# Optimization experiments

Measured on AMD Instinct MI355X. Metric: run time of the kernel, lower is better.

## Reference

```python
import jax, jax.numpy as jnp
import numpy as np

B, T, DIN, H = 32, 4096, 256, 256


def _log_g(x):
    # log of g(x) = where(x>=0, x+0.5, sigmoid(x)), computed stably in log space
    return jnp.where(x >= 0.0, jnp.log(jax.nn.relu(x) + 0.5), -jax.nn.softplus(-x))


def setup_inputs() -> dict:
    key = jax.random.key(0)
    ks = jax.random.split(key, 4)
    scale = (6.0 / (DIN + H)) ** 0.5  # xavier_uniform
    return {
        "x": jax.random.normal(ks[0], (B, T, DIN), dtype=jnp.float32),
        "h0": jax.random.normal(ks[1], (B, 1, H), dtype=jnp.float32),
        "Wz": jax.random.uniform(ks[2], (H, DIN), jnp.float32, -scale, scale),
        "bz": jnp.zeros((H,), jnp.float32),
        "Wh": jax.random.uniform(ks[3], (H, DIN), jnp.float32, -scale, scale),
        "bh": jnp.zeros((H,), jnp.float32),
    }


def reference(x, h0, Wz, bz, Wh, bh):
    # minGRU training path: log-space parallel scan (Heinsen scan)
    k = jnp.einsum("bti,hi->bth", x, Wz) + bz            # pre-activation of z gate
    log_z = -jax.nn.softplus(-k)                           # log sigmoid(k)
    log_coeffs = -jax.nn.softplus(k)                       # log(1 - sigmoid(k))
    log_h0 = _log_g(h0)                                    # (B,1,H)
    log_tilde_h = _log_g(jnp.einsum("bti,hi->bth", x, Wh) + bh)
    log_values = jnp.concatenate([log_h0, log_z + log_tilde_h], axis=1)  # (B,T+1,H)
    # a_star[t] = sum_{s<=t} log_coeffs[s], with a leading zero
    a_star = jnp.cumsum(jnp.pad(log_coeffs, ((0, 0), (1, 0), (0, 0))), axis=1)
    # logcumsumexp along time via associative scan with logaddexp
    lcse = jax.lax.associative_scan(jnp.logaddexp, log_values - a_star, axis=1)
    log_h = a_star + lcse                                  # (B,T+1,H)
    return jnp.exp(log_h[:, 1:])                           # (B,T,H)
```

## Files before the change

kernel.cpp:

```cpp
#include <hip/hip_runtime.h>
#include <hip/hip_fp16.h>

typedef __attribute__((ext_vector_type(8))) short short8;
typedef __attribute__((ext_vector_type(4))) float f32x4;
typedef unsigned short ushort_t;
typedef unsigned int uint_t;

#define B_SZ 32
#define T_SZ 4096
#define D_IN 256
#define H_SZ 256
#define M_SZ (B_SZ * T_SZ)
#define CHUNK 64
#define NCHUNK (T_SZ / CHUNK)

__device__ __forceinline__ ushort_t f2bf(float f) {
  unsigned int u = __float_as_uint(f);
  unsigned int r = (u + 0x7FFFu + ((u >> 16) & 1u)) >> 16;
  return (ushort_t)r;
}

__device__ __forceinline__ float sigmoidf_(float xv) {
  float e = __expf(-fabsf(xv));
  float s = 1.0f / (1.0f + e);
  return xv >= 0.0f ? s : 1.0f - s;
}

__device__ __forceinline__ float unpack_lo(uint_t pk) {
  return __half2float(__ushort_as_half((ushort_t)(pk & 0xFFFFu)));
}
__device__ __forceinline__ float unpack_hi(uint_t pk) {
  return __half2float(__ushort_as_half((ushort_t)(pk >> 16)));
}

__global__ void prep_w(const float* __restrict__ Wz, const float* __restrict__ Wh,
                       ushort_t* __restrict__ wsB) {
  int g = blockIdx.x * 256 + threadIdx.x;
  if (g >= 8 * 2048) return;
  int ks = g >> 11;
  int r = g & 2047;
  int c = r >> 9;
  int n = r & 511;
  int h = (n >> 5) * 16 + (n & 15);
  const float* W = ((n >> 4) & 1) ? Wh : Wz;
  const float* src = W + (size_t)h * D_IN + ks * 32 + c * 8;
  ushort_t* dst = wsB + (size_t)g * 8;
#pragma unroll
  for (int j = 0; j < 8; ++j) dst[j] = f2bf(src[j]);
}

__global__ __launch_bounds__(512, 4) void gemm_av(
    const float* __restrict__ x, const ushort_t* __restrict__ wsB,
    const float* __restrict__ bz, const float* __restrict__ bh,
    uint_t* __restrict__ av) {
  __shared__ __align__(16) unsigned char lds[73728];
  ushort_t* As = (ushort_t*)lds;
  ushort_t* Bs = (ushort_t*)(lds + 8192);

  const int tid = threadIdx.x;
  const int lane = tid & 63;
  const int wid = tid >> 6;
  const int m0 = blockIdx.x * 64;

  const int a_row = tid & 63;
  const int a_g = tid >> 6;
  const float* asrc = x + (size_t)(m0 + a_row) * D_IN + a_g * 8;

  f32x4 acc[4][4];
#pragma unroll
  for (int rt = 0; rt < 4; ++rt)
#pragma unroll
    for (int ct = 0; ct < 4; ++ct) {
      f32x4 z4 = {0.f, 0.f, 0.f, 0.f};
      acc[rt][ct] = z4;
    }

  {
    const ushort_t* bsrc = wsB + (size_t)wid * 2048 + lane * 8;
    ushort_t* bdst = Bs + wid * 2048;
#pragma unroll
    for (int cc = 0; cc < 4; ++cc) {
      __builtin_amdgcn_global_load_lds(
          (const __attribute__((address_space(1))) void*)(bsrc + cc * 512),
          (__attribute__((address_space(3))) void*)(bdst + cc * 512), 16, 0, 0);
    }
    if (tid < 256) {
      float4 f0 = *(const float4*)(asrc);
      float4 f1 = *(const float4*)(asrc + 4);
      short8 vfr;
      ushort_t* vp = (ushort_t*)&vfr;
      vp[0] = f2bf(f0.x); vp[1] = f2bf(f0.y); vp[2] = f2bf(f0.z); vp[3] = f2bf(f0.w);
      vp[4] = f2bf(f1.x); vp[5] = f2bf(f1.y); vp[6] = f2bf(f1.z); vp[7] = f2bf(f1.w);
      *(short8*)(As + tid * 8) = vfr;
    }
  }
  __syncthreads();

#pragma unroll
  for (int ks = 0; ks < 8; ++ks) {
    const int cur = ks & 1;
    short8 afr[4], bfr[4];
    {
      const int c = lane >> 4;
      const int r16 = lane & 15;
#pragma unroll
      for (int rt = 0; rt < 4; ++rt) {
        int row = rt * 16 + r16;
        afr[rt] = *(const short8*)(As + cur * 2048 + (c * 64 + row) * 8);
      }
#pragma unroll
      for (int ct = 0; ct < 4; ++ct) {
        int n = wid * 64 + ct * 16 + r16;
        bfr[ct] = *(const short8*)(Bs + cur * 16384 + (c * 512 + n) * 8);
      }
    }
    float4 nf0, nf1;
    if (ks < 7) {
      const ushort_t* bsrc = wsB + (size_t)(ks + 1) * 16384 + wid * 2048 + lane * 8;
      ushort_t* bdst = Bs + (cur ^ 1) * 16384 + wid * 2048;
#pragma unroll
      for (int cc = 0; cc < 4; ++cc) {
        __builtin_amdgcn_global_load_lds(
            (const __attribute__((address_space(1))) void*)(bsrc + cc * 512),
            (__attribute__((address_space(3))) void*)(bdst + cc * 512), 16, 0, 0);
      }
      if (tid < 256) {
        nf0 = *(const float4*)(asrc + (ks + 1) * 32);
        nf1 = *(const float4*)(asrc + (ks + 1) * 32 + 4);
      }
    }
#pragma unroll
    for (int rt = 0; rt < 4; ++rt)
#pragma unroll
      for (int ct = 0; ct < 4; ++ct)
        acc[rt][ct] = __builtin_amdgcn_mfma_f32_16x16x32_bf16(
            afr[rt], bfr[ct], acc[rt][ct], 0, 0, 0);
    if (ks < 7 && tid < 256) {
      short8 vfr;
      ushort_t* vp = (ushort_t*)&vfr;
      vp[0] = f2bf(nf0.x); vp[1] = f2bf(nf0.y); vp[2] = f2bf(nf0.z); vp[3] = f2bf(nf0.w);
      vp[4] = f2bf(nf1.x); vp[5] = f2bf(nf1.y); vp[6] = f2bf(nf1.z); vp[7] = f2bf(nf1.w);
      *(short8*)(As + (cur ^ 1) * 2048 + tid * 8) = vfr;
    }
    __syncthreads();
  }

  const int col16 = lane & 15;
  const int rgrp = lane >> 4;
#pragma unroll
  for (int i = 0; i < 2; ++i) {
    int hh = (wid * 2 + i) * 16 + col16;
    float bzv = bz[hh];
    float bhv = bh[hh];
#pragma unroll
    for (int rt = 0; rt < 4; ++rt) {
#pragma unroll
      for (int j = 0; j < 4; ++j) {
        int row = m0 + rt * 16 + rgrp * 4 + j;
        float kv = acc[rt][2 * i][j] + bzv;
        float pv = acc[rt][2 * i + 1][j] + bhv;
        float a = sigmoidf_(-kv);
        float z = 1.0f - a;
        float gg = (pv >= 0.0f) ? (pv + 0.5f) : sigmoidf_(pv);
        float vv = z * gg;
        uint_t pk = (uint_t)__half_as_ushort(__float2half_rn(a)) |
                    ((uint_t)__half_as_ushort(__float2half_rn(vv)) << 16);
        av[(size_t)row * H_SZ + hh] = pk;
      }
    }
  }
}

__global__ __launch_bounds__(256) void chunk_reduce(
    const uint_t* __restrict__ av, float2* __restrict__ cAV) {
  const int b = blockIdx.x >> 6;
  const int c = blockIdx.x & 63;
  const int h = threadIdx.x;
  const uint_t* p = av + ((size_t)b * T_SZ + c * CHUNK) * H_SZ + h;

  uint_t buf[CHUNK];
#pragma unroll
  for (int s = 0; s < CHUNK; ++s) buf[s] = p[(size_t)s * H_SZ];

  float A = 1.0f, V = 0.0f;
#pragma unroll
  for (int s = 0; s < CHUNK; ++s) {
    float a = unpack_lo(buf[s]);
    float v = unpack_hi(buf[s]);
    A = a * A;
    V = fmaf(a, V, v);
  }
  float2 r; r.x = A; r.y = V;
  cAV[((size_t)b * NCHUNK + c) * H_SZ + h] = r;
}

__global__ __launch_bounds__(256) void chunk_carry(
    const float* __restrict__ h0, const float2* __restrict__ cAV,
    float* __restrict__ hb) {
  const int b = blockIdx.x;
  const int h = threadIdx.x;
  float v0 = h0[b * H_SZ + h];
  float hc = (v0 >= 0.0f) ? (v0 + 0.5f) : sigmoidf_(v0);

  const float2* p = cAV + (size_t)b * NCHUNK * H_SZ + h;
  float* o = hb + (size_t)b * NCHUNK * H_SZ + h;

  float2 buf[NCHUNK];
#pragma unroll
  for (int c = 0; c < NCHUNK; ++c) buf[c] = p[(size_t)c * H_SZ];

#pragma unroll
  for (int c = 0; c < NCHUNK; ++c) {
    o[(size_t)c * H_SZ] = hc;
    hc = fmaf(buf[c].x, hc, buf[c].y);
  }
}

__global__ __launch_bounds__(256) void chunk_scan_out(
    const uint_t* av, const float* __restrict__ hb, float* out) {
  const int b = blockIdx.x >> 6;
  const int c = blockIdx.x & 63;
  const int h = threadIdx.x;

  float hc = hb[((size_t)b * NCHUNK + c) * H_SZ + h];
  const uint_t* p = av + ((size_t)b * T_SZ + c * CHUNK) * H_SZ + h;
  float* o = out + ((size_t)b * T_SZ + c * CHUNK) * H_SZ + h;

  uint_t buf[CHUNK];
#pragma unroll
  for (int s = 0; s < CHUNK; ++s) buf[s] = p[(size_t)s * H_SZ];

#pragma unroll
  for (int s = 0; s < CHUNK; ++s) {
    float a = unpack_lo(buf[s]);
    float v = unpack_hi(buf[s]);
    hc = fmaf(a, hc, v);
    o[(size_t)s * H_SZ] = hc;
  }
}

__global__ __launch_bounds__(64) void scan_seq(const float* __restrict__ h0,
                                               const uint_t* av, float* out) {
  const int b = blockIdx.x >> 2;
  const int hg = blockIdx.x & 3;
  const int h = hg * 64 + threadIdx.x;

  float v0 = h0[b * H_SZ + h];
  float hc = (v0 >= 0.0f) ? (v0 + 0.5f) : sigmoidf_(v0);

  const uint_t* p = av + (size_t)b * T_SZ * H_SZ + h;
  float* o = out + (size_t)b * T_SZ * H_SZ + h;

  uint_t buf[32];
#pragma unroll
  for (int d = 0; d < 32; ++d) buf[d] = p[(size_t)d * H_SZ];

  for (int t0 = 0; t0 < T_SZ; t0 += 32) {
#pragma unroll
    for (int d = 0; d < 32; ++d) {
      int t = t0 + d;
      uint_t pk = buf[d];
      int tn = t + 32;
      if (tn < T_SZ) buf[d] = p[(size_t)tn * H_SZ];
      hc = fmaf(unpack_lo(pk), hc, unpack_hi(pk));
      o[(size_t)t * H_SZ] = hc;
    }
  }
}

extern "C" void kernel_launch(void* const* d_in, const int* in_sizes, int n_in,
                              void* d_out, int out_size, void* d_ws, size_t ws_size,
                              hipStream_t stream) {
  const float* x  = (const float*)d_in[0];
  const float* h0 = (const float*)d_in[1];
  const float* Wz = (const float*)d_in[2];
  const float* bz = (const float*)d_in[3];
  const float* Wh = (const float*)d_in[4];
  const float* bh = (const float*)d_in[5];
  float* out = (float*)d_out;

  const size_t wsBBytes = 262144;
  const size_t cavBytes = (size_t)B_SZ * NCHUNK * H_SZ * 8;
  const size_t hbBytes  = (size_t)B_SZ * NCHUNK * H_SZ * 4;
  const size_t avOff    = 8388608;
  const size_t avBytes  = (size_t)M_SZ * H_SZ * 4;

  ushort_t* wsB = (ushort_t*)d_ws;
  float2* cAV = (float2*)((char*)d_ws + wsBBytes);
  float* hb   = (float*)((char*)d_ws + wsBBytes + cavBytes);

  const bool haveSummaries = ws_size >= wsBBytes + cavBytes + hbBytes;
  uint_t* av;
  if (ws_size >= avOff + avBytes) {
    av = (uint_t*)((char*)d_ws + avOff);
  } else {
    av = (uint_t*)d_out;
  }

  prep_w<<<64, 256, 0, stream>>>(Wz, Wh, wsB);
  gemm_av<<<M_SZ / 64, 512, 0, stream>>>(x, wsB, bz, bh, av);
  if (haveSummaries) {
    chunk_reduce<<<B_SZ * NCHUNK, 256, 0, stream>>>(av, cAV);
    chunk_carry<<<B_SZ, 256, 0, stream>>>(h0, cAV, hb);
    chunk_scan_out<<<B_SZ * NCHUNK, 256, 0, stream>>>(av, hb, out);
  } else {
    scan_seq<<<B_SZ * 4, 64, 0, stream>>>(h0, av, out);
  }
}
```

Baseline: 174.7 us.

## Keep weights in registers and stream fp32 x tiles via swizzled LDS

The GEMM kernel now loads each wave's full bf16 weight slice into registers once per block and processes four 64-row chunks per block, so the weight tile is no longer restaged through LDS for every 64-row tile. Raw fp32 x rows are copied straight into a double-buffered, XOR-swizzled LDS buffer with global_load_lds, and the bf16 conversion happens at fragment-read time. prep_w is relaid out to match the per-lane register fragment order. This cuts weight traffic and per-tile setup, at the cost of heavy register use (occupancy hint lowered to 2), 128KB of LDS per block, and redundant conversion of x per wave.

```diff
diff --git a/kernel.cpp b/kernel.cpp
--- a/kernel.cpp
+++ b/kernel.cpp
@@ -13,6 +13,8 @@
 #define M_SZ (B_SZ * T_SZ)
 #define CHUNK 64
 #define NCHUNK (T_SZ / CHUNK)
+#define NC_PER_BLK 4
+#define GEMM_GRID (M_SZ / (NC_PER_BLK * CHUNK))
 
 __device__ __forceinline__ ushort_t f2bf(float f) {
   unsigned int u = __float_as_uint(f);
@@ -36,138 +38,126 @@
 __global__ void prep_w(const float* __restrict__ Wz, const float* __restrict__ Wh,
                        ushort_t* __restrict__ wsB) {
   int g = blockIdx.x * 256 + threadIdx.x;
-  if (g >= 8 * 2048) return;
-  int ks = g >> 11;
-  int r = g & 2047;
-  int c = r >> 9;
-  int n = r & 511;
-  int h = (n >> 5) * 16 + (n & 15);
-  const float* W = ((n >> 4) & 1) ? Wh : Wz;
-  const float* src = W + (size_t)h * D_IN + ks * 32 + c * 8;
+  if (g >= 32 * 8 * 64) return;
+  int lane = g & 63;
+  int ks = (g >> 6) & 7;
+  int grp = g >> 9;
+  int c16 = lane & 15;
+  int h = (grp >> 1) * 16 + c16;
+  int k0 = ks * 32 + (lane >> 4) * 8;
+  const float* W = (grp & 1) ? Wh : Wz;
+  const float* src = W + (size_t)h * D_IN + k0;
   ushort_t* dst = wsB + (size_t)g * 8;
 #pragma unroll
   for (int j = 0; j < 8; ++j) dst[j] = f2bf(src[j]);
 }
 
-__global__ __launch_bounds__(512, 4) void gemm_av(
+__global__ __launch_bounds__(512, 2) void gemm_av(
     const float* __restrict__ x, const ushort_t* __restrict__ wsB,
     const float* __restrict__ bz, const float* __restrict__ bh,
     uint_t* __restrict__ av) {
-  __shared__ __align__(16) unsigned char lds[73728];
-  ushort_t* As = (ushort_t*)lds;
-  ushort_t* Bs = (ushort_t*)(lds + 8192);
+  __shared__ __align__(16) float ldsA[2 * CHUNK * D_IN];
 
   const int tid = threadIdx.x;
   const int lane = tid & 63;
   const int wid = tid >> 6;
-  const int m0 = blockIdx.x * 64;
-
-  const int a_row = tid & 63;
-  const int a_g = tid >> 6;
-  const float* asrc = x + (size_t)(m0 + a_row) * D_IN + a_g * 8;
-
-  f32x4 acc[4][4];
-#pragma unroll
-  for (int rt = 0; rt < 4; ++rt)
-#pragma unroll
-    for (int ct = 0; ct < 4; ++ct) {
-      f32x4 z4 = {0.f, 0.f, 0.f, 0.f};
-      acc[rt][ct] = z4;
-    }
-
-  {
-    const ushort_t* bsrc = wsB + (size_t)wid * 2048 + lane * 8;
-    ushort_t* bdst = Bs + wid * 2048;
-#pragma unroll
-    for (int cc = 0; cc < 4; ++cc) {
-      __builtin_amdgcn_global_load_lds(
-          (const __attribute__((address_space(1))) void*)(bsrc + cc * 512),
-          (__attribute__((address_space(3))) void*)(bdst + cc * 512), 16, 0, 0);
-    }
-    if (tid < 256) {
-      float4 f0 = *(const float4*)(asrc);
-      float4 f1 = *(const float4*)(asrc + 4);
-      short8 vfr;
-      ushort_t* vp = (ushort_t*)&vfr;
-      vp[0] = f2bf(f0.x); vp[1] = f2bf(f0.y); vp[2] = f2bf(f0.z); vp[3] = f2bf(f0.w);
-      vp[4] = f2bf(f1.x); vp[5] = f2bf(f1.y); vp[6] = f2bf(f1.z); vp[7] = f2bf(f1.w);
-      *(short8*)(As + tid * 8) = vfr;
-    }
-  }
-  __syncthreads();
-
-#pragma unroll
-  for (int ks = 0; ks < 8; ++ks) {
-    const int cur = ks & 1;
-    short8 afr[4], bfr[4];
-    {
-      const int c = lane >> 4;
-      const int r16 = lane & 15;
-#pragma unroll
-      for (int rt = 0; rt < 4; ++rt) {
-        int row = rt * 16 + r16;
-        afr[rt] = *(const short8*)(As + cur * 2048 + (c * 64 + row) * 8);
-      }
-#pragma unroll
-      for (int ct = 0; ct < 4; ++ct) {
-        int n = wid * 64 + ct * 16 + r16;
-        bfr[ct] = *(const short8*)(Bs + cur * 16384 + (c * 512 + n) * 8);
-      }
-    }
-    float4 nf0, nf1;
-    if (ks < 7) {
-      const ushort_t* bsrc = wsB + (size_t)(ks + 1) * 16384 + wid * 2048 + lane * 8;
-      ushort_t* bdst = Bs + (cur ^ 1) * 16384 + wid * 2048;
-#pragma unroll
-      for (int cc = 0; cc < 4; ++cc) {
-        __builtin_amdgcn_global_load_lds(
-            (const __attribute__((address_space(1))) void*)(bsrc + cc * 512),
-            (__attribute__((address_space(3))) void*)(bdst + cc * 512), 16, 0, 0);
-      }
-      if (tid < 256) {
-        nf0 = *(const float4*)(asrc + (ks + 1) * 32);
-        nf1 = *(const float4*)(asrc + (ks + 1) * 32 + 4);
-      }
-    }
-#pragma unroll
-    for (int rt = 0; rt < 4; ++rt)
-#pragma unroll
-      for (int ct = 0; ct < 4; ++ct)
-        acc[rt][ct] = __builtin_amdgcn_mfma_f32_16x16x32_bf16(
-            afr[rt], bfr[ct], acc[rt][ct], 0, 0, 0);
-    if (ks < 7 && tid < 256) {
-      short8 vfr;
-      ushort_t* vp = (ushort_t*)&vfr;
-      vp[0] = f2bf(nf0.x); vp[1] = f2bf(nf0.y); vp[2] = f2bf(nf0.z); vp[3] = f2bf(nf0.w);
-      vp[4] = f2bf(nf1.x); vp[5] = f2bf(nf1.y); vp[6] = f2bf(nf1.z); vp[7] = f2bf(nf1.w);
-      *(short8*)(As + (cur ^ 1) * 2048 + tid * 8) = vfr;
-    }
-    __syncthreads();
-  }
-
   const int col16 = lane & 15;
   const int rgrp = lane >> 4;
+  const size_t rowBase = (size_t)blockIdx.x * (NC_PER_BLK * CHUNK);
+
+  short8 bfr[4][8];
+#pragma unroll
+  for (int ct = 0; ct < 4; ++ct)
+#pragma unroll
+    for (int ks = 0; ks < 8; ++ks)
+      bfr[ct][ks] =
+          *(const short8*)(wsB + ((size_t)(((wid * 4 + ct) * 8 + ks) * 64 + lane)) * 8);
+
+  float bzv[2], bhv[2];
 #pragma unroll
   for (int i = 0; i < 2; ++i) {
     int hh = (wid * 2 + i) * 16 + col16;
-    float bzv = bz[hh];
-    float bhv = bh[hh];
-#pragma unroll
-    for (int rt = 0; rt < 4; ++rt) {
-#pragma unroll
-      for (int j = 0; j < 4; ++j) {
-        int row = m0 + rt * 16 + rgrp * 4 + j;
-        float kv = acc[rt][2 * i][j] + bzv;
-        float pv = acc[rt][2 * i + 1][j] + bhv;
-        float a = sigmoidf_(-kv);
-        float z = 1.0f - a;
-        float gg = (pv >= 0.0f) ? (pv + 0.5f) : sigmoidf_(pv);
-        float vv = z * gg;
-        uint_t pk = (uint_t)__half_as_ushort(__float2half_rn(a)) |
-                    ((uint_t)__half_as_ushort(__float2half_rn(vv)) << 16);
-        av[(size_t)row * H_SZ + hh] = pk;
+    bzv[i] = bz[hh];
+    bhv[i] = bh[hh];
+  }
+
+  auto STAGE = [&](int cc) {
+    const char* xbase = (const char*)(x + (rowBase + (size_t)cc * CHUNK) * D_IN);
+    const int soff = (lane * 16) ^ (wid << 4);
+    char* lbase = (char*)&ldsA[(cc & 1) * (CHUNK * D_IN)];
+#pragma unroll
+    for (int q = 0; q < 8; ++q) {
+      const int r = q * 8 + wid;
+      __builtin_amdgcn_global_load_lds(
+          (const __attribute__((address_space(1))) void*)(xbase + (size_t)r * 1024 + soff),
+          (__attribute__((address_space(3))) void*)(lbase + r * 1024), 16, 0, 0);
+    }
+  };
+
+  STAGE(0);
+  __syncthreads();
+
+  const int koffsw = (rgrp * 32) ^ ((lane & 7) << 4);
+
+#pragma unroll 1
+  for (int cc = 0; cc < NC_PER_BLK; ++cc) {
+    if (cc + 1 < NC_PER_BLK) STAGE(cc + 1);
+
+    const char* Ab = (const char*)&ldsA[(cc & 1) * (CHUNK * D_IN)];
+
+    f32x4 acc[4][4];
+#pragma unroll
+    for (int rt = 0; rt < 4; ++rt)
+#pragma unroll
+      for (int ct = 0; ct < 4; ++ct) {
+        f32x4 z4 = {0.f, 0.f, 0.f, 0.f};
+        acc[rt][ct] = z4;
       }
-    }
+
+#pragma unroll
+    for (int ks = 0; ks < 8; ++ks) {
+#pragma unroll
+      for (int rt = 0; rt < 4; ++rt) {
+        const int row = rt * 16 + col16;
+        const int a1 = row * 1024 + ks * 128 + koffsw;
+        float4 f0 = *(const float4*)(Ab + a1);
+        float4 f1 = *(const float4*)(Ab + (a1 ^ 16));
+        union { ushort_t e[8]; short8 s; } cv;
+        cv.e[0] = f2bf(f0.x); cv.e[1] = f2bf(f0.y);
+        cv.e[2] = f2bf(f0.z); cv.e[3] = f2bf(f0.w);
+        cv.e[4] = f2bf(f1.x); cv.e[5] = f2bf(f1.y);
+        cv.e[6] = f2bf(f1.z); cv.e[7] = f2bf(f1.w);
+        short8 afr = cv.s;
+#pragma unroll
+        for (int ct = 0; ct < 4; ++ct)
+          acc[rt][ct] = __builtin_amdgcn_mfma_f32_16x16x32_bf16(
+              afr, bfr[ct][ks], acc[rt][ct], 0, 0, 0);
+      }
+    }
+
+    const size_t crow0 = rowBase + (size_t)cc * CHUNK;
+#pragma unroll
+    for (int i = 0; i < 2; ++i) {
+      const int hh = (wid * 2 + i) * 16 + col16;
+#pragma unroll
+      for (int rt = 0; rt < 4; ++rt) {
+#pragma unroll
+        for (int j = 0; j < 4; ++j) {
+          float kv = acc[rt][2 * i][j] + bzv[i];
+          float pv = acc[rt][2 * i + 1][j] + bhv[i];
+          float a = sigmoidf_(-kv);
+          float z = 1.0f - a;
+          float gg = (pv >= 0.0f) ? (pv + 0.5f) : sigmoidf_(pv);
+          float vv = z * gg;
+          int row = rt * 16 + rgrp * 4 + j;
+          uint_t pk = (uint_t)__half_as_ushort(__float2half_rn(a)) |
+                      ((uint_t)__half_as_ushort(__float2half_rn(vv)) << 16);
+          av[(crow0 + row) * H_SZ + hh] = pk;
+        }
+      }
+    }
+
+    __syncthreads();
   }
 }
 
@@ -298,7 +288,7 @@
   }
 
   prep_w<<<64, 256, 0, stream>>>(Wz, Wh, wsB);
-  gemm_av<<<M_SZ / 64, 512, 0, stream>>>(x, wsB, bz, bh, av);
+  gemm_av<<<GEMM_GRID, 512, 0, stream>>>(x, wsB, bz, bh, av);
   if (haveSummaries) {
     chunk_reduce<<<B_SZ * NCHUNK, 256, 0, stream>>>(av, cAV);
     chunk_carry<<<B_SZ, 256, 0, stream>>>(h0, cAV, hb);
```

After: 186.6 us. 1.07x slower.

## Load pre-swizzled weight fragments directly into registers instead of staging through LDS

Applied to the files above, without the earlier changes.

The weight prep kernel now writes the bf16 weights in MFMA fragment order per wave, lane and k-step. The GEMM kernel then reads each B fragment with one coalesced 16-byte global load straight into registers, double-buffered across k-steps. This removes the 64KB LDS B buffer and the LDS read traffic, shrinking shared memory from 72KB to 8KB so more blocks can be resident. The cost is that every block re-fetches weights from L2 through the vector path and uses more registers per thread.

```diff
diff --git a/kernel.cpp b/kernel.cpp
--- a/kernel.cpp
+++ b/kernel.cpp
@@ -36,14 +36,15 @@
 __global__ void prep_w(const float* __restrict__ Wz, const float* __restrict__ Wh,
                        ushort_t* __restrict__ wsB) {
   int g = blockIdx.x * 256 + threadIdx.x;
-  if (g >= 8 * 2048) return;
-  int ks = g >> 11;
-  int r = g & 2047;
-  int c = r >> 9;
-  int n = r & 511;
-  int h = (n >> 5) * 16 + (n & 15);
-  const float* W = ((n >> 4) & 1) ? Wh : Wz;
-  const float* src = W + (size_t)h * D_IN + ks * 32 + c * 8;
+  if (g >= 32 * 8 * 64) return;
+  int lane = g & 63;
+  int ks = (g >> 6) & 7;
+  int grp = g >> 9;
+  int c16 = lane & 15;
+  int h = (grp >> 1) * 16 + c16;
+  int k0 = ks * 32 + (lane >> 4) * 8;
+  const float* W = (grp & 1) ? Wh : Wz;
+  const float* src = W + (size_t)h * D_IN + k0;
   ushort_t* dst = wsB + (size_t)g * 8;
 #pragma unroll
   for (int j = 0; j < 8; ++j) dst[j] = f2bf(src[j]);
@@ -53,9 +54,8 @@
     const float* __restrict__ x, const ushort_t* __restrict__ wsB,
     const float* __restrict__ bz, const float* __restrict__ bh,
     uint_t* __restrict__ av) {
-  __shared__ __align__(16) unsigned char lds[73728];
+  __shared__ __align__(16) unsigned char lds[8192];
   ushort_t* As = (ushort_t*)lds;
-  ushort_t* Bs = (ushort_t*)(lds + 8192);
 
   const int tid = threadIdx.x;
   const int lane = tid & 63;
@@ -66,6 +66,8 @@
   const int a_g = tid >> 6;
   const float* asrc = x + (size_t)(m0 + a_row) * D_IN + a_g * 8;
 
+  const short8* bgr = (const short8*)wsB;
+
   f32x4 acc[4][4];
 #pragma unroll
   for (int rt = 0; rt < 4; ++rt)
@@ -75,23 +77,21 @@
       acc[rt][ct] = z4;
     }
 
+  short8 bfr[2][4];
+
   {
-    const ushort_t* bsrc = wsB + (size_t)wid * 2048 + lane * 8;
-    ushort_t* bdst = Bs + wid * 2048;
-#pragma unroll
-    for (int cc = 0; cc < 4; ++cc) {
-      __builtin_amdgcn_global_load_lds(
-          (const __attribute__((address_space(1))) void*)(bsrc + cc * 512),
-          (__attribute__((address_space(3))) void*)(bdst + cc * 512), 16, 0, 0);
-    }
+#pragma unroll
+    for (int ct = 0; ct < 4; ++ct)
+      bfr[0][ct] = bgr[((wid * 4 + ct) * 8 + 0) * 64 + lane];
     if (tid < 256) {
       float4 f0 = *(const float4*)(asrc);
       float4 f1 = *(const float4*)(asrc + 4);
-      short8 vfr;
-      ushort_t* vp = (ushort_t*)&vfr;
-      vp[0] = f2bf(f0.x); vp[1] = f2bf(f0.y); vp[2] = f2bf(f0.z); vp[3] = f2bf(f0.w);
-      vp[4] = f2bf(f1.x); vp[5] = f2bf(f1.y); vp[6] = f2bf(f1.z); vp[7] = f2bf(f1.w);
-      *(short8*)(As + tid * 8) = vfr;
+      union { ushort_t e[8]; short8 s; } cv;
+      cv.e[0] = f2bf(f0.x); cv.e[1] = f2bf(f0.y);
+      cv.e[2] = f2bf(f0.z); cv.e[3] = f2bf(f0.w);
+      cv.e[4] = f2bf(f1.x); cv.e[5] = f2bf(f1.y);
+      cv.e[6] = f2bf(f1.z); cv.e[7] = f2bf(f1.w);
+      *(short8*)(As + tid * 8) = cv.s;
     }
   }
   __syncthreads();
@@ -99,7 +99,7 @@
 #pragma unroll
   for (int ks = 0; ks < 8; ++ks) {
     const int cur = ks & 1;
-    short8 afr[4], bfr[4];
+    short8 afr[4];
     {
       const int c = lane >> 4;
       const int r16 = lane & 15;
@@ -108,22 +108,12 @@
         int row = rt * 16 + r16;
         afr[rt] = *(const short8*)(As + cur * 2048 + (c * 64 + row) * 8);
       }
-#pragma unroll
-      for (int ct = 0; ct < 4; ++ct) {
-        int n = wid * 64 + ct * 16 + r16;
-        bfr[ct] = *(const short8*)(Bs + cur * 16384 + (c * 512 + n) * 8);
-      }
     }
     float4 nf0, nf1;
     if (ks < 7) {
-      const ushort_t* bsrc = wsB + (size_t)(ks + 1) * 16384 + wid * 2048 + lane * 8;
-      ushort_t* bdst = Bs + (cur ^ 1) * 16384 + wid * 2048;
-#pragma unroll
-      for (int cc = 0; cc < 4; ++cc) {
-        __builtin_amdgcn_global_load_lds(
-            (const __attribute__((address_space(1))) void*)(bsrc + cc * 512),
-            (__attribute__((address_space(3))) void*)(bdst + cc * 512), 16, 0, 0);
-      }
+#pragma unroll
+      for (int ct = 0; ct < 4; ++ct)
+        bfr[cur ^ 1][ct] = bgr[((wid * 4 + ct) * 8 + (ks + 1)) * 64 + lane];
       if (tid < 256) {
         nf0 = *(const float4*)(asrc + (ks + 1) * 32);
         nf1 = *(const float4*)(asrc + (ks + 1) * 32 + 4);
@@ -134,13 +124,14 @@
 #pragma unroll
       for (int ct = 0; ct < 4; ++ct)
         acc[rt][ct] = __builtin_amdgcn_mfma_f32_16x16x32_bf16(
-            afr[rt], bfr[ct], acc[rt][ct], 0, 0, 0);
+            afr[rt], bfr[cur][ct], acc[rt][ct], 0, 0, 0);
     if (ks < 7 && tid < 256) {
-      short8 vfr;
-      ushort_t* vp = (ushort_t*)&vfr;
-      vp[0] = f2bf(nf0.x); vp[1] = f2bf(nf0.y); vp[2] = f2bf(nf0.z); vp[3] = f2bf(nf0.w);
-      vp[4] = f2bf(nf1.x); vp[5] = f2bf(nf1.y); vp[6] = f2bf(nf1.z); vp[7] = f2bf(nf1.w);
-      *(short8*)(As + (cur ^ 1) * 2048 + tid * 8) = vfr;
+      union { ushort_t e[8]; short8 s; } cv;
+      cv.e[0] = f2bf(nf0.x); cv.e[1] = f2bf(nf0.y);
+      cv.e[2] = f2bf(nf0.z); cv.e[3] = f2bf(nf0.w);
+      cv.e[4] = f2bf(nf1.x); cv.e[5] = f2bf(nf1.y);
+      cv.e[6] = f2bf(nf1.z); cv.e[7] = f2bf(nf1.w);
+      *(short8*)(As + (cur ^ 1) * 2048 + tid * 8) = cv.s;
     }
     __syncthreads();
   }
```

Measured after the change: 203.3 us. 1.16x slower.
